# Performance work log

Measured on AMD Instinct MI355X. Metric: run time of the kernel, lower is better.

The kernel has to match this reference:

```python
import jax, jax.numpy as jnp
import numpy as np

N_E = 1024
E_DIM = 256
BETA = 0.25
EMA_LAMBDA = 0.99

def setup_inputs() -> dict:
    key = jax.random.key(0)
    k1, k2 = jax.random.split(key)
    z = jax.random.normal(k1, (32, 2048, E_DIM), dtype=jnp.float32)
    # torch init: uniform(-1/n_e, 1/n_e)
    embedding = jax.random.uniform(k2, (N_E, E_DIM), dtype=jnp.float32,
                                   minval=-1.0 / N_E, maxval=1.0 / N_E)
    N_t = jnp.zeros((N_E,), dtype=jnp.float32)
    m_t = jnp.zeros((N_E, E_DIM), dtype=jnp.float32)
    return {"z": z, "embedding": embedding, "N_t": N_t, "m_t": m_t}

def reference(z, embedding, N_t, m_t):
    zf = z.reshape(-1, E_DIM)  # [N, e_dim]
    # squared L2 distances: ||z||^2 + ||e||^2 - 2 z e^T  -> [N, n_e]
    d = (jnp.sum(zf * zf, axis=1, keepdims=True)
         + jnp.sum(embedding * embedding, axis=1)
         - 2.0 * jnp.matmul(zf, embedding.T))
    idx = jnp.argmin(d, axis=1)  # [N] int

    # EMA statistics (torch does a python loop over unique indices; this is the
    # vectorized equivalent: only codes that were selected get updated).
    counts = jax.ops.segment_sum(jnp.ones_like(idx, dtype=jnp.float32), idx, num_segments=N_E)
    sums = jax.ops.segment_sum(zf, idx, num_segments=N_E)  # [n_e, e_dim]
    selected = counts > 0
    N_t_new = jnp.where(selected, N_t * EMA_LAMBDA + counts * (1.0 - EMA_LAMBDA), N_t)
    m_t_new = jnp.where(selected[:, None], m_t * EMA_LAMBDA + sums * (1.0 - EMA_LAMBDA), m_t)

    z_q = embedding[idx].reshape(z.shape)
    loss = BETA * jnp.mean((jax.lax.stop_gradient(z_q) - z) ** 2)
    z_q_st = z + jax.lax.stop_gradient(z_q - z)  # straight-through

    # perplexity from code usage histogram (== mean of one-hot encodings)
    e_mean = counts / idx.shape[0]
    perplexity = jnp.exp(-jnp.sum(e_mean * jnp.log(e_mean + 1e-10)))
    return (loss, z_q_st, idx, perplexity, N_t_new, m_t_new)
```

## Files before the change

### kernel.cpp

```cpp
#include <hip/hip_runtime.h>
#include <math.h>

#define N_ROWS  65536
#define EDIM    256
#define NE      1024
#define BETA    0.25f
#define LAMBDA  0.99f

#define MARGIN  8e-3f
#define QCAP    2048


#define O_ZQ   1
#define O_IDX  16777217
#define O_PERP 16842753
#define O_NT   16842754
#define O_MT   16843778

typedef __attribute__((ext_vector_type(8))) short short8;
typedef __attribute__((ext_vector_type(4))) float f32x4;

__device__ __forceinline__ unsigned short f2bf(float f) {
    unsigned u = __float_as_uint(f);
    return (unsigned short)((u + 0x7fffu + ((u >> 16) & 1u)) >> 16);
}

__global__ __launch_bounds__(64) void prep_b_kernel(const float* __restrict__ emb,
                                                    unsigned* __restrict__ bfrag_u32,
                                                    float* __restrict__ loss_acc,
                                                    int* __restrict__ cnt) {
    int j = blockIdx.x;
    int l = threadIdx.x;
    float4 v = ((const float4*)(emb + (size_t)j * EDIM))[l];
    unsigned lo = (unsigned)f2bf(v.x) | ((unsigned)f2bf(v.y) << 16);
    unsigned hi = (unsigned)f2bf(v.z) | ((unsigned)f2bf(v.w) << 16);
    int base = ((((j >> 4) * 8 + (l >> 3)) * 64) + ((l >> 1) & 3) * 16 + (j & 15)) * 4
             + 2 * (l & 1);
    bfrag_u32[base]     = lo;
    bfrag_u32[base + 1] = hi;
    if (l == 0) cnt[j] = 0;
    if (j == 0 && l == 0) *loss_acc = 0.0f;
}

__global__ __launch_bounds__(256) void sq_kernel(const float* __restrict__ src,
                                                 float* __restrict__ dst) {
    const int tid = threadIdx.x;
    const int grp = tid >> 4;
    const int q   = tid & 15;
    const int row = blockIdx.x * 16 + grp;
    const int h = q >> 3, j = q & 7;
    const float* __restrict__ p = src + (size_t)row * EDIM + h * 128 + j;
    float acc = __fmul_rn(p[0], p[0]);
    #pragma unroll
    for (int t = 1; t < 16; ++t) {
        float v = p[8 * t];
        acc = __fadd_rn(acc, __fmul_rn(v, v));
    }
    acc = __fadd_rn(acc, __shfl_xor(acc, 1));
    acc = __fadd_rn(acc, __shfl_xor(acc, 2));
    acc = __fadd_rn(acc, __shfl_xor(acc, 4));
    acc = __fadd_rn(acc, __shfl_xor(acc, 8));
    if (q == 0) dst[row] = acc;
}

__global__ __launch_bounds__(256, 3) void argmin_kernel(const float* __restrict__ z,
                                                        const float* __restrict__ emb,
                                                        const float4* __restrict__ bsrc,
                                                        const float* __restrict__ e_sq,
                                                        int* __restrict__ idx_out,
                                                        float* __restrict__ out_zq,
                                                        float* __restrict__ out_idx,
                                                        float* __restrict__ loss_acc,
                                                        int* __restrict__ cnt) {
    __shared__ __align__(16) float4 Bs[2048];
    __shared__ uint2 queue[QCAP];
    __shared__ unsigned long long best_s[64];
    __shared__ int   idx_s[64];
    __shared__ float zsq_s[64];
    __shared__ float rmF_s[64];
    __shared__ int qcnt;

    const int tid  = threadIdx.x;
    const int wid  = tid >> 6, lane = tid & 63;
    const int l15  = lane & 15, lg = lane >> 4;
    const int row0 = blockIdx.x * 64;
    const int rbase = row0 + wid * 16;

    if (tid < 64) best_s[tid] = ~0ull;
    if (tid == 0) qcnt = 0;

    float4 st[8];
    #pragma unroll
    for (int i = 0; i < 8; ++i) st[i] = bsrc[tid + 256 * i];

    short8 a[8];
    {
        float zs = 0.f;
        #pragma unroll
        for (int ks = 0; ks < 8; ++ks) {
            const float* zp = z + (size_t)(rbase + l15) * EDIM + ks * 32 + lg * 8;
            float4 f0 = *(const float4*)zp;
            float4 f1 = *(const float4*)(zp + 4);
            zs += f0.x * f0.x + f0.y * f0.y + f0.z * f0.z + f0.w * f0.w
                + f1.x * f1.x + f1.y * f1.y + f1.z * f1.z + f1.w * f1.w;
            union { short8 s; unsigned short u[8]; } pk;
            pk.u[0] = f2bf(f0.x); pk.u[1] = f2bf(f0.y); pk.u[2] = f2bf(f0.z); pk.u[3] = f2bf(f0.w);
            pk.u[4] = f2bf(f1.x); pk.u[5] = f2bf(f1.y); pk.u[6] = f2bf(f1.z); pk.u[7] = f2bf(f1.w);
            a[ks] = pk.s;
        }
        zs += __shfl_xor(zs, 16);
        zs += __shfl_xor(zs, 32);
        if (lg == 0) zsq_s[wid * 16 + l15] = zs;
    }

    float rm[4];
    #pragma unroll
    for (int r = 0; r < 4; ++r) rm[r] = 1e30f;

    __syncthreads();

    for (int ch = 0; ch < 16; ++ch) {
        const int cb = ch * 64;
        #pragma unroll
        for (int i = 0; i < 8; ++i) Bs[tid + 256 * i] = st[i];
        __syncthreads();
        if (ch < 15) {
            #pragma unroll
            for (int i = 0; i < 8; ++i) st[i] = bsrc[(ch + 1) * 2048 + tid + 256 * i];
        }

        float eqs[4];
        #pragma unroll
        for (int ct = 0; ct < 4; ++ct) eqs[ct] = e_sq[cb + ct * 16 + l15];

        f32x4 acc[4];
        #pragma unroll
        for (int ct = 0; ct < 4; ++ct) acc[ct] = (f32x4){0.f, 0.f, 0.f, 0.f};

        const short8* Bv = (const short8*)Bs;
        #pragma unroll
        for (int ks = 0; ks < 8; ++ks) {
            #pragma unroll
            for (int ct = 0; ct < 4; ++ct) {
                short8 b = Bv[(ct * 8 + ks) * 64 + lane];
                acc[ct] = __builtin_amdgcn_mfma_f32_16x16x32_bf16(a[ks], b, acc[ct], 0, 0, 0);
            }
        }

        #pragma unroll
        for (int r = 0; r < 4; ++r) {
            float m = __fsub_rn(eqs[0], __fmul_rn(2.0f, acc[0][r]));
            #pragma unroll
            for (int ct = 1; ct < 4; ++ct) {
                float t = __fsub_rn(eqs[ct], __fmul_rn(2.0f, acc[ct][r]));
                m = fminf(m, t);
            }
            m = fminf(m, __shfl_xor(m, 1));
            m = fminf(m, __shfl_xor(m, 2));
            m = fminf(m, __shfl_xor(m, 4));
            m = fminf(m, __shfl_xor(m, 8));
            rm[r] = fminf(rm[r], m);
        }

        #pragma unroll
        for (int ct = 0; ct < 4; ++ct) {
            #pragma unroll
            for (int r = 0; r < 4; ++r) {
                float t = __fsub_rn(eqs[ct], __fmul_rn(2.0f, acc[ct][r]));
                if (t <= rm[r] + MARGIN) {
                    int rl  = wid * 16 + lg * 4 + r;
                    int col = cb + ct * 16 + l15;
                    int s = atomicAdd(&qcnt, 1);
                    if (s < QCAP) queue[s] = make_uint2((rl << 10) | col,
                                                        __float_as_uint(t));
                }
            }
        }
        __syncthreads();
    }

    #pragma unroll
    for (int r = 0; r < 4; ++r)
        if (l15 == 0) rmF_s[wid * 16 + lg * 4 + r] = rm[r];
    __syncthreads();

    {
        int nq = qcnt; if (nq > QCAP) nq = QCAP;
        const int g = tid >> 3, q = tid & 7;
        for (int e = g; e < nq; e += 32) {
            uint2 ent = queue[e];
            int rl = ent.x >> 10, col = ent.x & 1023;
            if (__uint_as_float(ent.y) > rmF_s[rl] + MARGIN) continue;
            const float4* zr = (const float4*)(z + (size_t)(row0 + rl) * EDIM);
            const float4* er = (const float4*)(emb + (size_t)col * EDIM);
            float ae = 0.f;
            #pragma unroll
            for (int i = 0; i < 8; ++i) {
                float4 x = zr[q + 8 * i], y = er[q + 8 * i];
                ae = __fmaf_rn(x.x, y.x, ae);
                ae = __fmaf_rn(x.y, y.y, ae);
                ae = __fmaf_rn(x.z, y.z, ae);
                ae = __fmaf_rn(x.w, y.w, ae);
            }
            ae = __fadd_rn(ae, __shfl_xor(ae, 1));
            ae = __fadd_rn(ae, __shfl_xor(ae, 2));
            ae = __fadd_rn(ae, __shfl_xor(ae, 4));
            if (q == 0) {
                float d = __fsub_rn(__fadd_rn(zsq_s[rl], e_sq[col]), __fmul_rn(2.0f, ae));
                unsigned u = __float_as_uint(d);
                u = (u & 0x80000000u) ? ~u : (u | 0x80000000u);
                unsigned long long key = ((unsigned long long)u << 32) | (unsigned)col;
                atomicMin(&best_s[rl], key);
            }
        }
    }

    __syncthreads();
    if (tid < 64) {
        unsigned long long k = best_s[tid];
        int id = (int)(k & 0xffffffffull);
        idx_out[row0 + tid] = id;
        out_idx[row0 + tid] = (float)id;
        idx_s[tid] = id;
        atomicAdd(&cnt[id], 1);
    }
    __syncthreads();

    for (int i = 0; i < 64; ++i) {
        int id = idx_s[i];
        out_zq[(size_t)(row0 + i) * EDIM + tid] = emb[(size_t)id * EDIM + tid];
    }

    if (wid == 0) {
        unsigned m = (unsigned)(best_s[lane] >> 32);
        unsigned bits = (m & 0x80000000u) ? (m & 0x7fffffffu) : ~m;
        float lp = __uint_as_float(bits);
        #pragma unroll
        for (int mm = 32; mm; mm >>= 1) lp += __shfl_down(lp, mm);
        if (lane == 0) atomicAdd(loss_acc, lp);
    }
}

__global__ __launch_bounds__(1024) void scan_kernel(const int* __restrict__ cnt,
                                                    const float* __restrict__ N_t,
                                                    float* __restrict__ outN,
                                                    float* __restrict__ counts_f,
                                                    int* __restrict__ offs,
                                                    int* __restrict__ cursor) {
    __shared__ int s[1024];
    const int tid = threadIdx.x;
    int c = cnt[tid];
    s[tid] = c;
    __syncthreads();
    for (int d = 1; d < 1024; d <<= 1) {
        int v = (tid >= d) ? s[tid - d] : 0;
        __syncthreads();
        s[tid] += v;
        __syncthreads();
    }
    int excl = s[tid] - c;
    offs[tid] = excl;
    cursor[tid] = excl;
    counts_f[tid] = (float)c;
    float Nold = N_t[tid];
    outN[tid] = (c > 0) ? Nold * LAMBDA + (float)c * (1.0f - LAMBDA) : Nold;
}

__global__ __launch_bounds__(256) void scatter_kernel(const int* __restrict__ idx,
                                                      int* __restrict__ cursor,
                                                      int* __restrict__ sorted) {
    int i = blockIdx.x * 256 + threadIdx.x;
    int p = atomicAdd(&cursor[idx[i]], 1);
    sorted[p] = i;
}

__global__ __launch_bounds__(512) void msum_kernel(const float* __restrict__ z,
                                                   const int* __restrict__ sorted,
                                                   const int* __restrict__ offs,
                                                   const int* __restrict__ cnt,
                                                   const float* __restrict__ m_t,
                                                   float* __restrict__ outM) {
    const int j = blockIdx.x;
    const int tid = threadIdx.x, w = tid >> 6, lane = tid & 63;
    const int n = cnt[j], start = offs[j];
    float4 acc = make_float4(0.f, 0.f, 0.f, 0.f);
    for (int e = w; e < n; e += 8) {
        float4 v = ((const float4*)(z + (size_t)sorted[start + e] * EDIM))[lane];
        acc.x += v.x; acc.y += v.y; acc.z += v.z; acc.w += v.w;
    }
    __shared__ float red[8 * 256];
    *(float4*)(red + w * 256 + lane * 4) = acc;
    __syncthreads();
    if (tid < 256) {
        float s = 0.f;
        #pragma unroll
        for (int ww = 0; ww < 8; ++ww) s += red[ww * 256 + tid];
        float mold = m_t[(size_t)j * EDIM + tid];
        outM[(size_t)j * EDIM + tid] = (n > 0) ? mold * LAMBDA + s * (1.0f - LAMBDA) : mold;
    }
}

__global__ __launch_bounds__(256) void final_kernel(const float* __restrict__ counts,
                                                    const float* __restrict__ loss_acc,
                                                    float* __restrict__ out_loss,
                                                    float* __restrict__ out_perp) {
    const int tid = threadIdx.x, w = tid >> 6, lane = tid & 63;
    float h = 0.f;
    for (int c = tid; c < NE; c += 256) {
        float em = counts[c] * (1.0f / (float)N_ROWS);
        h += em * logf(em + 1e-10f);
    }
    #pragma unroll
    for (int m = 32; m; m >>= 1) h += __shfl_down(h, m);
    __shared__ float red[4];
    if (lane == 0) red[w] = h;
    __syncthreads();
    if (tid == 0) {
        float H = red[0] + red[1] + red[2] + red[3];
        out_perp[0] = expf(-H);
        out_loss[0] = BETA * loss_acc[0] * (1.0f / (float)(N_ROWS * EDIM));
    }
}

extern "C" void kernel_launch(void* const* d_in, const int* in_sizes, int n_in,
                              void* d_out, int out_size, void* d_ws, size_t ws_size,
                              hipStream_t stream) {
    const float* z   = (const float*)d_in[0];
    const float* emb = (const float*)d_in[1];
    const float* N_t = (const float*)d_in[2];
    const float* m_t = (const float*)d_in[3];
    float* out = (float*)d_out;
    float* ws  = (float*)d_ws;

    float* loss_acc   = ws;
    float* e_sq       = ws + 64;
    unsigned* bfrag_u = (unsigned*)(ws + 67584);
    int*   sorted     = (int*)(ws + 198656);
    int*   idx1       = (int*)(ws + 264192);
    float* counts     = ws + 329728;
    int*   cnt_i      = (int*)(ws + 330752);
    int*   offs_i     = (int*)(ws + 331776);
    int*   cursor_i   = (int*)(ws + 332800);

    prep_b_kernel<<<NE, 64, 0, stream>>>(emb, bfrag_u, loss_acc, cnt_i);
    sq_kernel<<<NE / 16, 256, 0, stream>>>(emb, e_sq);
    argmin_kernel<<<N_ROWS / 64, 256, 0, stream>>>(z, emb, (const float4*)bfrag_u,
                                                   e_sq, idx1,
                                                   out + O_ZQ, out + O_IDX, loss_acc, cnt_i);
    scan_kernel<<<1, 1024, 0, stream>>>(cnt_i, N_t, out + O_NT, counts, offs_i, cursor_i);
    scatter_kernel<<<N_ROWS / 256, 256, 0, stream>>>(idx1, cursor_i, sorted);
    msum_kernel<<<NE, 512, 0, stream>>>(z, sorted, offs_i, cnt_i, m_t, out + O_MT);
    final_kernel<<<1, 256, 0, stream>>>(counts, loss_acc, out, out + O_PERP);
}
```

Measured before the change: 367.6 us.

## Double-buffer codebook tiles via direct global-to-LDS loads and vectorize z_q gather

Replaces the register-staged codebook copy with global_load_lds transfers into a two-buffer LDS ring, halving the chunk to 32 codes so both buffers fit, and prefetches the next chunk while the current one is used by MFMA. This aims to cut register pressure and VGPR-to-LDS store traffic and to overlap loads with compute. The candidate queue shrinks to 1024 entries, which risks overflow dropping candidates. The z_q gather now reads float4 but writes scalars because out_zq is offset by one float. Correctness depends on the async LDS load completing before the barrier, which the code does not wait for explicitly.

Measured after the change: 316.3 us. -13.9%, faster.

```diff
diff --git a/kernel.cpp b/kernel.cpp
--- a/kernel.cpp
+++ b/kernel.cpp
@@ -8,7 +8,7 @@
 #define LAMBDA  0.99f
 
 #define MARGIN  8e-3f
-#define QCAP    2048
+#define QCAP    1024
 
 
 #define O_ZQ   1
@@ -72,7 +72,7 @@
                                                         float* __restrict__ out_idx,
                                                         float* __restrict__ loss_acc,
                                                         int* __restrict__ cnt) {
-    __shared__ __align__(16) float4 Bs[2048];
+    __shared__ __align__(16) float4 Bs[2][1024];
     __shared__ uint2 queue[QCAP];
     __shared__ unsigned long long best_s[64];
     __shared__ int   idx_s[64];
@@ -89,9 +89,16 @@
     if (tid < 64) best_s[tid] = ~0ull;
     if (tid == 0) qcnt = 0;
 
-    float4 st[8];
-    #pragma unroll
-    for (int i = 0; i < 8; ++i) st[i] = bsrc[tid + 256 * i];
+    {
+        const char* g = (const char*)bsrc + wid * 4096 + lane * 16;
+        char* l = (char*)&Bs[0][0] + wid * 4096;
+        #pragma unroll
+        for (int i = 0; i < 4; ++i)
+            __builtin_amdgcn_global_load_lds(
+                (const __attribute__((address_space(1))) unsigned int*)(g + i * 1024),
+                (__attribute__((address_space(3))) unsigned int*)(l + i * 1024),
+                16, 0, 0);
+    }
 
     short8 a[8];
     {
@@ -119,29 +126,34 @@
 
     __syncthreads();
 
-    for (int ch = 0; ch < 16; ++ch) {
-        const int cb = ch * 64;
-        #pragma unroll
-        for (int i = 0; i < 8; ++i) Bs[tid + 256 * i] = st[i];
-        __syncthreads();
-        if (ch < 15) {
+    int buf = 0;
+    for (int ch = 0; ch < 32; ++ch) {
+        const int cb = ch * 32;
+
+        if (ch < 31) {
+            const char* g = (const char*)bsrc + (ch + 1) * 16384 + wid * 4096 + lane * 16;
+            char* l = (char*)&Bs[buf ^ 1][0] + wid * 4096;
             #pragma unroll
-            for (int i = 0; i < 8; ++i) st[i] = bsrc[(ch + 1) * 2048 + tid + 256 * i];
-        }
-
-        float eqs[4];
-        #pragma unroll
-        for (int ct = 0; ct < 4; ++ct) eqs[ct] = e_sq[cb + ct * 16 + l15];
-
-        f32x4 acc[4];
-        #pragma unroll
-        for (int ct = 0; ct < 4; ++ct) acc[ct] = (f32x4){0.f, 0.f, 0.f, 0.f};
-
-        const short8* Bv = (const short8*)Bs;
+            for (int i = 0; i < 4; ++i)
+                __builtin_amdgcn_global_load_lds(
+                    (const __attribute__((address_space(1))) unsigned int*)(g + i * 1024),
+                    (__attribute__((address_space(3))) unsigned int*)(l + i * 1024),
+                    16, 0, 0);
+        }
+
+        float eqs[2];
+        #pragma unroll
+        for (int ct = 0; ct < 2; ++ct) eqs[ct] = e_sq[cb + ct * 16 + l15];
+
+        f32x4 acc[2];
+        #pragma unroll
+        for (int ct = 0; ct < 2; ++ct) acc[ct] = (f32x4){0.f, 0.f, 0.f, 0.f};
+
+        const short8* Bv = (const short8*)&Bs[buf][0];
         #pragma unroll
         for (int ks = 0; ks < 8; ++ks) {
             #pragma unroll
-            for (int ct = 0; ct < 4; ++ct) {
+            for (int ct = 0; ct < 2; ++ct) {
                 short8 b = Bv[(ct * 8 + ks) * 64 + lane];
                 acc[ct] = __builtin_amdgcn_mfma_f32_16x16x32_bf16(a[ks], b, acc[ct], 0, 0, 0);
             }
@@ -149,12 +161,9 @@
 
         #pragma unroll
         for (int r = 0; r < 4; ++r) {
-            float m = __fsub_rn(eqs[0], __fmul_rn(2.0f, acc[0][r]));
-            #pragma unroll
-            for (int ct = 1; ct < 4; ++ct) {
-                float t = __fsub_rn(eqs[ct], __fmul_rn(2.0f, acc[ct][r]));
-                m = fminf(m, t);
-            }
+            float m0 = __fsub_rn(eqs[0], __fmul_rn(2.0f, acc[0][r]));
+            float t1 = __fsub_rn(eqs[1], __fmul_rn(2.0f, acc[1][r]));
+            float m = fminf(m0, t1);
             m = fminf(m, __shfl_xor(m, 1));
             m = fminf(m, __shfl_xor(m, 2));
             m = fminf(m, __shfl_xor(m, 4));
@@ -163,7 +172,7 @@
         }
 
         #pragma unroll
-        for (int ct = 0; ct < 4; ++ct) {
+        for (int ct = 0; ct < 2; ++ct) {
             #pragma unroll
             for (int r = 0; r < 4; ++r) {
                 float t = __fsub_rn(eqs[ct], __fmul_rn(2.0f, acc[ct][r]));
@@ -176,7 +185,9 @@
                 }
             }
         }
+
         __syncthreads();
+        buf ^= 1;
     }
 
     #pragma unroll
@@ -226,9 +237,14 @@
     }
     __syncthreads();
 
-    for (int i = 0; i < 64; ++i) {
-        int id = idx_s[i];
-        out_zq[(size_t)(row0 + i) * EDIM + tid] = emb[(size_t)id * EDIM + tid];
+    const float4* e4 = (const float4*)emb;
+    for (int i = 0; i < 16; ++i) {
+        int flat = tid + i * 256;
+        int r = flat >> 6, c4 = flat & 63;
+        int id = idx_s[r];
+        float4 e = e4[(size_t)id * 64 + c4];
+        float* o = out_zq + (size_t)(row0 + r) * EDIM + c4 * 4;
+        o[0] = e.x; o[1] = e.y; o[2] = e.z; o[3] = e.w;
     }
 
     if (wid == 0) {
```

## Split codebook across waves, stream B fragments from global, drop per-chunk barriers

Applied to the files above, without the earlier changes.

The argmin kernel now gives each block 32 rows. All four waves share the same rows and each wave scans its own quarter of the codebook, loading the bf16 B fragments straight from global/L2 into registers instead of staging them through LDS with a barrier per chunk. MFMA operands are swapped so codebook columns map to the accumulator registers, which shortens the cross-lane min reduction. Per-wave running minima are merged in shared memory before refinement, e_sq is cached in LDS, and the z_q gather is vectorized. The trade-off is more global B traffic (each block rereads the whole codebook for half as many rows) and twice as many blocks. The per-wave minima are also looser thresholds early on, so more candidates may be queued.

After: 318.9 us. 1.15x faster.

```diff
diff --git a/kernel.cpp b/kernel.cpp
--- a/kernel.cpp
+++ b/kernel.cpp
@@ -65,40 +65,39 @@
 
 __global__ __launch_bounds__(256, 3) void argmin_kernel(const float* __restrict__ z,
                                                         const float* __restrict__ emb,
-                                                        const float4* __restrict__ bsrc,
+                                                        const short8* __restrict__ bfrag,
                                                         const float* __restrict__ e_sq,
                                                         int* __restrict__ idx_out,
                                                         float* __restrict__ out_zq,
                                                         float* __restrict__ out_idx,
                                                         float* __restrict__ loss_acc,
                                                         int* __restrict__ cnt) {
-    __shared__ __align__(16) float4 Bs[2048];
+    __shared__ float e_lds[NE];
     __shared__ uint2 queue[QCAP];
-    __shared__ unsigned long long best_s[64];
-    __shared__ int   idx_s[64];
-    __shared__ float zsq_s[64];
-    __shared__ float rmF_s[64];
-    __shared__ int qcnt;
-
-    const int tid  = threadIdx.x;
-    const int wid  = tid >> 6, lane = tid & 63;
-    const int l15  = lane & 15, lg = lane >> 4;
-    const int row0 = blockIdx.x * 64;
-    const int rbase = row0 + wid * 16;
-
-    if (tid < 64) best_s[tid] = ~0ull;
+    __shared__ unsigned long long best_s[32];
+    __shared__ float rmW_s[4][32];
+    __shared__ float rmF_s[32];
+    __shared__ float zsq_s[32];
+    __shared__ int   idx_s[32];
+    __shared__ int   qcnt;
+
+    const int tid = threadIdx.x;
+    const int wid = tid >> 6, lane = tid & 63;
+    const int l15 = lane & 15, lg = lane >> 4;
+    const int row0 = blockIdx.x * 32;
+
+    if (tid < 32) best_s[tid] = ~0ull;
     if (tid == 0) qcnt = 0;
-
-    float4 st[8];
-    #pragma unroll
-    for (int i = 0; i < 8; ++i) st[i] = bsrc[tid + 256 * i];
-
-    short8 a[8];
-    {
+    #pragma unroll
+    for (int i = 0; i < 4; ++i) e_lds[tid + 256 * i] = e_sq[tid + 256 * i];
+
+    short8 a[2][8];
+    #pragma unroll
+    for (int rt = 0; rt < 2; ++rt) {
         float zs = 0.f;
         #pragma unroll
         for (int ks = 0; ks < 8; ++ks) {
-            const float* zp = z + (size_t)(rbase + l15) * EDIM + ks * 32 + lg * 8;
+            const float* zp = z + (size_t)(row0 + rt * 16 + l15) * EDIM + ks * 32 + lg * 8;
             float4 f0 = *(const float4*)zp;
             float4 f1 = *(const float4*)(zp + 4);
             zs += f0.x * f0.x + f0.y * f0.y + f0.z * f0.z + f0.w * f0.w
@@ -106,82 +105,61 @@
             union { short8 s; unsigned short u[8]; } pk;
             pk.u[0] = f2bf(f0.x); pk.u[1] = f2bf(f0.y); pk.u[2] = f2bf(f0.z); pk.u[3] = f2bf(f0.w);
             pk.u[4] = f2bf(f1.x); pk.u[5] = f2bf(f1.y); pk.u[6] = f2bf(f1.z); pk.u[7] = f2bf(f1.w);
-            a[ks] = pk.s;
+            a[rt][ks] = pk.s;
         }
         zs += __shfl_xor(zs, 16);
         zs += __shfl_xor(zs, 32);
-        if (lg == 0) zsq_s[wid * 16 + l15] = zs;
-    }
-
-    float rm[4];
-    #pragma unroll
-    for (int r = 0; r < 4; ++r) rm[r] = 1e30f;
-
+        if (wid == rt && lg == 0) zsq_s[rt * 16 + l15] = zs;
+    }
+
+    float rm[2] = {1e30f, 1e30f};
     __syncthreads();
 
     for (int ch = 0; ch < 16; ++ch) {
-        const int cb = ch * 64;
-        #pragma unroll
-        for (int i = 0; i < 8; ++i) Bs[tid + 256 * i] = st[i];
-        __syncthreads();
-        if (ch < 15) {
+        const int cb = wid * 256 + ch * 16;
+        short8 b[8];
+        #pragma unroll
+        for (int ks = 0; ks < 8; ++ks)
+            b[ks] = bfrag[((size_t)(wid * 16 + ch) * 8 + ks) * 64 + lane];
+
+        f32x4 acc[2];
+        #pragma unroll
+        for (int rt = 0; rt < 2; ++rt) acc[rt] = (f32x4){0.f, 0.f, 0.f, 0.f};
+        #pragma unroll
+        for (int ks = 0; ks < 8; ++ks)
             #pragma unroll
-            for (int i = 0; i < 8; ++i) st[i] = bsrc[(ch + 1) * 2048 + tid + 256 * i];
+            for (int rt = 0; rt < 2; ++rt)
+                acc[rt] = __builtin_amdgcn_mfma_f32_16x16x32_bf16(b[ks], a[rt][ks], acc[rt], 0, 0, 0);
+
+        const float4 eq = ((const float4*)e_lds)[(cb >> 2) + lg];
+
+        #pragma unroll
+        for (int rt = 0; rt < 2; ++rt) {
+            float t0 = __fsub_rn(eq.x, __fmul_rn(2.0f, acc[rt][0]));
+            float t1 = __fsub_rn(eq.y, __fmul_rn(2.0f, acc[rt][1]));
+            float t2 = __fsub_rn(eq.z, __fmul_rn(2.0f, acc[rt][2]));
+            float t3 = __fsub_rn(eq.w, __fmul_rn(2.0f, acc[rt][3]));
+            float m = fminf(fminf(t0, t1), fminf(t2, t3));
+            m = fminf(m, __shfl_xor(m, 16));
+            m = fminf(m, __shfl_xor(m, 32));
+            rm[rt] = fminf(rm[rt], m);
+            const float thr = rm[rt] + MARGIN;
+            const int rl = rt * 16 + l15;
+            if (t0 <= thr) { int s = atomicAdd(&qcnt, 1); if (s < QCAP) queue[s] = make_uint2((rl << 10) | (cb + lg * 4 + 0), __float_as_uint(t0)); }
+            if (t1 <= thr) { int s = atomicAdd(&qcnt, 1); if (s < QCAP) queue[s] = make_uint2((rl << 10) | (cb + lg * 4 + 1), __float_as_uint(t1)); }
+            if (t2 <= thr) { int s = atomicAdd(&qcnt, 1); if (s < QCAP) queue[s] = make_uint2((rl << 10) | (cb + lg * 4 + 2), __float_as_uint(t2)); }
+            if (t3 <= thr) { int s = atomicAdd(&qcnt, 1); if (s < QCAP) queue[s] = make_uint2((rl << 10) | (cb + lg * 4 + 3), __float_as_uint(t3)); }
         }
-
-        float eqs[4];
-        #pragma unroll
-        for (int ct = 0; ct < 4; ++ct) eqs[ct] = e_sq[cb + ct * 16 + l15];
-
-        f32x4 acc[4];
-        #pragma unroll
-        for (int ct = 0; ct < 4; ++ct) acc[ct] = (f32x4){0.f, 0.f, 0.f, 0.f};
-
-        const short8* Bv = (const short8*)Bs;
-        #pragma unroll
-        for (int ks = 0; ks < 8; ++ks) {
-            #pragma unroll
-            for (int ct = 0; ct < 4; ++ct) {
-                short8 b = Bv[(ct * 8 + ks) * 64 + lane];
-                acc[ct] = __builtin_amdgcn_mfma_f32_16x16x32_bf16(a[ks], b, acc[ct], 0, 0, 0);
-            }
-        }
-
-        #pragma unroll
-        for (int r = 0; r < 4; ++r) {
-            float m = __fsub_rn(eqs[0], __fmul_rn(2.0f, acc[0][r]));
-            #pragma unroll
-            for (int ct = 1; ct < 4; ++ct) {
-                float t = __fsub_rn(eqs[ct], __fmul_rn(2.0f, acc[ct][r]));
-                m = fminf(m, t);
-            }
-            m = fminf(m, __shfl_xor(m, 1));
-            m = fminf(m, __shfl_xor(m, 2));
-            m = fminf(m, __shfl_xor(m, 4));
-            m = fminf(m, __shfl_xor(m, 8));
-            rm[r] = fminf(rm[r], m);
-        }
-
-        #pragma unroll
-        for (int ct = 0; ct < 4; ++ct) {
-            #pragma unroll
-            for (int r = 0; r < 4; ++r) {
-                float t = __fsub_rn(eqs[ct], __fmul_rn(2.0f, acc[ct][r]));
-                if (t <= rm[r] + MARGIN) {
-                    int rl  = wid * 16 + lg * 4 + r;
-                    int col = cb + ct * 16 + l15;
-                    int s = atomicAdd(&qcnt, 1);
-                    if (s < QCAP) queue[s] = make_uint2((rl << 10) | col,
-                                                        __float_as_uint(t));
-                }
-            }
-        }
-        __syncthreads();
-    }
-
-    #pragma unroll
-    for (int r = 0; r < 4; ++r)
-        if (l15 == 0) rmF_s[wid * 16 + lg * 4 + r] = rm[r];
+    }
+
+    if (lg == 0) {
+        rmW_s[wid][l15]      = rm[0];
+        rmW_s[wid][16 + l15] = rm[1];
+    }
+    __syncthreads();
+    if (tid < 32)
+        rmF_s[tid] = fminf(fminf(rmW_s[0][tid], rmW_s[1][tid]),
+                           fminf(rmW_s[2][tid], rmW_s[3][tid]));
     __syncthreads();
 
     {
@@ -206,7 +184,7 @@
             ae = __fadd_rn(ae, __shfl_xor(ae, 2));
             ae = __fadd_rn(ae, __shfl_xor(ae, 4));
             if (q == 0) {
-                float d = __fsub_rn(__fadd_rn(zsq_s[rl], e_sq[col]), __fmul_rn(2.0f, ae));
+                float d = __fsub_rn(__fadd_rn(zsq_s[rl], e_lds[col]), __fmul_rn(2.0f, ae));
                 unsigned u = __float_as_uint(d);
                 u = (u & 0x80000000u) ? ~u : (u | 0x80000000u);
                 unsigned long long key = ((unsigned long long)u << 32) | (unsigned)col;
@@ -216,9 +194,9 @@
     }
 
     __syncthreads();
-    if (tid < 64) {
+    if (tid < 32) {
         unsigned long long k = best_s[tid];
-        int id = (int)(k & 0xffffffffull);
+        int id = (int)(k & 1023u);
         idx_out[row0 + tid] = id;
         out_idx[row0 + tid] = (float)id;
         idx_s[tid] = id;
@@ -226,15 +204,24 @@
     }
     __syncthreads();
 
-    for (int i = 0; i < 64; ++i) {
-        int id = idx_s[i];
-        out_zq[(size_t)(row0 + i) * EDIM + tid] = emb[(size_t)id * EDIM + tid];
+    const float4* e4 = (const float4*)emb;
+    #pragma unroll
+    for (int i = 0; i < 8; ++i) {
+        int flat = tid + i * 256;
+        int r = flat >> 6, c4 = flat & 63;
+        int id = idx_s[r];
+        float4 e = e4[(size_t)id * 64 + c4];
+        float* o = out_zq + (size_t)(row0 + r) * EDIM + c4 * 4;
+        o[0] = e.x; o[1] = e.y; o[2] = e.z; o[3] = e.w;
     }
 
     if (wid == 0) {
-        unsigned m = (unsigned)(best_s[lane] >> 32);
-        unsigned bits = (m & 0x80000000u) ? (m & 0x7fffffffu) : ~m;
-        float lp = __uint_as_float(bits);
+        float lp = 0.f;
+        if (lane < 32) {
+            unsigned m = (unsigned)(best_s[lane] >> 32);
+            unsigned bits = (m & 0x80000000u) ? (m & 0x7fffffffu) : ~m;
+            lp = __uint_as_float(bits);
+        }
         #pragma unroll
         for (int mm = 32; mm; mm >>= 1) lp += __shfl_down(lp, mm);
         if (lane == 0) atomicAdd(loss_acc, lp);
@@ -344,7 +331,7 @@
 
     prep_b_kernel<<<NE, 64, 0, stream>>>(emb, bfrag_u, loss_acc, cnt_i);
     sq_kernel<<<NE / 16, 256, 0, stream>>>(emb, e_sq);
-    argmin_kernel<<<N_ROWS / 64, 256, 0, stream>>>(z, emb, (const float4*)bfrag_u,
+    argmin_kernel<<<N_ROWS / 32, 256, 0, stream>>>(z, emb, (const short8*)bfrag_u,
                                                    e_sq, idx1,
                                                    out + O_ZQ, out + O_IDX, loss_acc, cnt_i);
     scan_kernel<<<1, 1024, 0, stream>>>(cnt_i, N_t, out + O_NT, counts, offs_i, cursor_i);
```
